# Performance work log

Measured on AMD Instinct MI355X. Metric: run time of the kernel, lower is better.

The kernel has to match this reference:

```python
import jax, jax.numpy as jnp
import numpy as np

N_NODES = 50000
N_EDGES = 800000
D_IN = 96
D_OUT = 96
NEG_SLOPE = 0.2


def setup_inputs() -> dict:
    key = jax.random.key(0)
    k1, k2, k3, k4, k5 = jax.random.split(key, 5)
    x = jax.random.normal(k1, (N_NODES, D_IN), dtype=jnp.float32)
    W = jax.random.normal(k2, (D_IN, D_OUT), dtype=jnp.float32) * (1.0 / np.sqrt(D_IN))
    att_src = jax.random.normal(k3, (D_OUT,), dtype=jnp.float32) * 0.1
    att_dst = jax.random.normal(k4, (D_OUT,), dtype=jnp.float32) * 0.1
    bias = jnp.zeros((D_OUT,), dtype=jnp.float32)
    edge_index = jax.random.randint(k5, (2, N_EDGES), 0, N_NODES, dtype=jnp.int64)
    return {"x": x, "W": W, "att_src": att_src, "att_dst": att_dst,
            "bias": bias, "edge_index": edge_index}


def reference(x, W, att_src, att_dst, bias, edge_index):
    N = x.shape[0]
    # Linear transform: h = x W   [N, D_out]
    h = x @ W
    # PyG GATConv default add_self_loops=True
    loops = jnp.arange(N, dtype=edge_index.dtype)
    src = jnp.concatenate([edge_index[0], loops])  # message source j
    dst = jnp.concatenate([edge_index[1], loops])  # aggregation target i
    # Per-node attention halves, gathered per edge
    a_src = h @ att_src  # [N]
    a_dst = h @ att_dst  # [N]
    e = jax.nn.leaky_relu(a_src[src] + a_dst[dst], NEG_SLOPE)  # [E+N]
    # Segment softmax over edges sharing the same destination
    m = jax.ops.segment_max(e, dst, num_segments=N)  # every node has a self-loop
    e = jnp.exp(e - m[dst])
    denom = jax.ops.segment_sum(e, dst, num_segments=N)
    alpha = e / (denom[dst] + 1e-16)  # [E+N]
    # Weighted scatter-aggregate of source features
    out = jax.ops.segment_sum(h[src] * alpha[:, None], dst, num_segments=N)
    return jnp.tanh(out + bias)
```

## Files before the change

### kernel.cpp

```cpp
#include <hip/hip_runtime.h>
#include <hip/hip_bf16.h>
#include <cstdint>

#define N_NODES 50000
#define N_EDGES 800000
#define D 96
#define NEG_SLOPE 0.2f
#define R1ROWS 16
#define BUCKET 64
#define NXCD 8
#define DST_PER_PART (N_NODES / NXCD)

__global__ __launch_bounds__(384) void k1_gemm(
    const float* __restrict__ x, const float* __restrict__ W,
    __hip_bfloat16* __restrict__ hb) {
    __shared__ float Ws[D][D];
    __shared__ float xs[R1ROWS][D];
    const int tx = threadIdx.x, ty = threadIdx.y;
    const int t = ty * 96 + tx;
    const size_t row0 = (size_t)blockIdx.x * R1ROWS;

    {
        const float4* W4 = (const float4*)W;
        float4* Ws4 = (float4*)Ws;
#pragma unroll
        for (int i = 0; i < 6; ++i) Ws4[t + 384 * i] = W4[t + 384 * i];
        const float4* x4 = (const float4*)(x + row0 * D);
        ((float4*)xs)[t] = x4[t];
    }
    __syncthreads();

    float acc0 = 0.f, acc1 = 0.f, acc2 = 0.f, acc3 = 0.f;
#pragma unroll
    for (int k = 0; k < D; k += 4) {
        float4 xa = *(const float4*)&xs[ty][k];
        float4 xb = *(const float4*)&xs[ty + 4][k];
        float4 xc = *(const float4*)&xs[ty + 8][k];
        float4 xd = *(const float4*)&xs[ty + 12][k];
        float w0 = Ws[k][tx], w1 = Ws[k + 1][tx], w2 = Ws[k + 2][tx], w3 = Ws[k + 3][tx];
        acc0 += xa.x * w0 + xa.y * w1 + xa.z * w2 + xa.w * w3;
        acc1 += xb.x * w0 + xb.y * w1 + xb.z * w2 + xb.w * w3;
        acc2 += xc.x * w0 + xc.y * w1 + xc.z * w2 + xc.w * w3;
        acc3 += xd.x * w0 + xd.y * w1 + xd.z * w2 + xd.w * w3;
    }
    hb[(row0 + ty     ) * D + tx] = __float2bfloat16(acc0);
    hb[(row0 + ty + 4 ) * D + tx] = __float2bfloat16(acc1);
    hb[(row0 + ty + 8 ) * D + tx] = __float2bfloat16(acc2);
    hb[(row0 + ty + 12) * D + tx] = __float2bfloat16(acc3);
}

__global__ __launch_bounds__(256) void k1b_att(
    const __hip_bfloat16* __restrict__ hb, const float* __restrict__ att_src,
    const float* __restrict__ att_dst, float* __restrict__ a_src,
    float* __restrict__ a_dst, int* __restrict__ cnt) {
    const int lane = threadIdx.x & 63;
    const int row = (blockIdx.x * 256 + threadIdx.x) >> 6;
    if (row >= N_NODES) return;
    float s = 0.f, d = 0.f;
    if (lane < 48) {
        uint hv = ((const uint*)hb)[(size_t)row * 48 + lane];
        float h0 = __uint_as_float(hv << 16);
        float h1 = __uint_as_float(hv & 0xffff0000u);
        float2 as = *(const float2*)(att_src + lane * 2);
        float2 ad = *(const float2*)(att_dst + lane * 2);
        s = h0 * as.x + h1 * as.y;
        d = h0 * ad.x + h1 * ad.y;
    }
#pragma unroll
    for (int off = 32; off >= 1; off >>= 1) {
        s += __shfl_down(s, off);
        d += __shfl_down(d, off);
    }
    if (lane == 0) { a_src[row] = s; a_dst[row] = d; cnt[row] = 0; }
}

__global__ void k_bucket(const int* __restrict__ ei,
                         const float* __restrict__ a_src, const float* __restrict__ a_dst,
                         int* __restrict__ cnt, uint* __restrict__ bkt) {
    const int part = blockIdx.x & (NXCD - 1);
    const int e = (blockIdx.x >> 3) * 256 + threadIdx.x;
    if (e >= N_EDGES) return;
    int d = ei[N_EDGES + e];
    int lo = part * DST_PER_PART;
    if (d < lo || d >= lo + DST_PER_PART) return;
    int s = ei[e];
    float v = a_src[s] + a_dst[d];
    v = v > 0.f ? v : NEG_SLOPE * v;
    float w = __expf(v);
    uint u = __float_as_uint(w);
    uint wb = (u + 0x7FFFu + ((u >> 16) & 1u)) & 0xFFFF0000u;
    uint pk = wb | (uint)s;
    int pos = atomicAdd(&cnt[d], 1);
    if (pos < BUCKET) bkt[(size_t)d * BUCKET + pos] = pk;
}

__global__ __launch_bounds__(256) void k_gather(
    const int* __restrict__ cnt, const uint* __restrict__ bkt,
    const float* __restrict__ a_src, const float* __restrict__ a_dst,
    const __hip_bfloat16* __restrict__ hb, const float* __restrict__ bias,
    float* __restrict__ out) {
    const uint lane = threadIdx.x & 63;
    const uint ll = (lane < 48u) ? lane : (lane - 16u);
    const int part = blockIdx.x & (NXCD - 1);
    const int l = (int)((blockIdx.x >> 3) * 4 + (threadIdx.x >> 6));
    if (l >= DST_PER_PART) return;
    const int node = part * DST_PER_PART + l;
    const uint* __restrict__ hbu = (const uint*)hb;
    const uint* __restrict__ bucket = bkt + (size_t)node * BUCKET;
    const int cn = min(cnt[node], BUCKET);

    float es = a_src[node] + a_dst[node];
    es = es > 0.f ? es : NEG_SLOPE * es;
    float wself = __expf(es);
    uint pself = hbu[(uint)node * 48u + ll];
    float acc0 = __uint_as_float(pself << 16) * wself;
    float acc1 = __uint_as_float(pself & 0xffff0000u) * wself;
    float wsum = wself;

    int k = 0;
    for (; k + 15 < cn; k += 16) {
        uint b[16];
        *(uint4*)&b[0]  = *(const uint4*)&bucket[k];
        *(uint4*)&b[4]  = *(const uint4*)&bucket[k + 4];
        *(uint4*)&b[8]  = *(const uint4*)&bucket[k + 8];
        *(uint4*)&b[12] = *(const uint4*)&bucket[k + 12];
        uint p[16];
#pragma unroll
        for (int j = 0; j < 16; ++j) p[j] = hbu[(b[j] & 0xFFFFu) * 48u + ll];
#pragma unroll
        for (int j = 0; j < 16; ++j) {
            float w = __uint_as_float(b[j] & 0xFFFF0000u);
            acc0 += __uint_as_float(p[j] << 16) * w;
            acc1 += __uint_as_float(p[j] & 0xffff0000u) * w;
            wsum += w;
        }
    }
    if (k + 7 < cn) {
        uint b[8];
        *(uint4*)&b[0] = *(const uint4*)&bucket[k];
        *(uint4*)&b[4] = *(const uint4*)&bucket[k + 4];
        uint p[8];
#pragma unroll
        for (int j = 0; j < 8; ++j) p[j] = hbu[(b[j] & 0xFFFFu) * 48u + ll];
#pragma unroll
        for (int j = 0; j < 8; ++j) {
            float w = __uint_as_float(b[j] & 0xFFFF0000u);
            acc0 += __uint_as_float(p[j] << 16) * w;
            acc1 += __uint_as_float(p[j] & 0xffff0000u) * w;
            wsum += w;
        }
        k += 8;
    }
    if (k + 3 < cn) {
        uint b[4];
        *(uint4*)&b[0] = *(const uint4*)&bucket[k];
        uint p[4];
#pragma unroll
        for (int j = 0; j < 4; ++j) p[j] = hbu[(b[j] & 0xFFFFu) * 48u + ll];
#pragma unroll
        for (int j = 0; j < 4; ++j) {
            float w = __uint_as_float(b[j] & 0xFFFF0000u);
            acc0 += __uint_as_float(p[j] << 16) * w;
            acc1 += __uint_as_float(p[j] & 0xffff0000u) * w;
            wsum += w;
        }
        k += 4;
    }
    for (; k < cn; ++k) {
        uint e0 = bucket[k];
        uint p0 = hbu[(e0 & 0xFFFFu) * 48u + ll];
        float w0 = __uint_as_float(e0 & 0xFFFF0000u);
        acc0 += __uint_as_float(p0 << 16) * w0;
        acc1 += __uint_as_float(p0 & 0xffff0000u) * w0;
        wsum += w0;
    }

    if (lane < 48) {
        float inv = 1.f / (wsum + 1e-16f);
        float2 bv = *(const float2*)(bias + lane * 2);
        float2 o;
        o.x = tanhf(acc0 * inv + bv.x);
        o.y = tanhf(acc1 * inv + bv.y);
        *(float2*)(out + (size_t)node * D + lane * 2) = o;
    }
}

extern "C" void kernel_launch(void* const* d_in, const int* in_sizes, int n_in,
                              void* d_out, int out_size, void* d_ws, size_t ws_size,
                              hipStream_t stream) {
    const float* x       = (const float*)d_in[0];
    const float* W       = (const float*)d_in[1];
    const float* att_src = (const float*)d_in[2];
    const float* att_dst = (const float*)d_in[3];
    const float* bias    = (const float*)d_in[4];
    const int*   ei      = (const int*)d_in[5];
    float* out = (float*)d_out;

    char* ws = (char*)d_ws;
    __hip_bfloat16* hb = (__hip_bfloat16*)ws; ws += (size_t)N_NODES * D * 2;
    float* a_src  = (float*)ws; ws += (size_t)N_NODES * 4;
    float* a_dst  = (float*)ws; ws += (size_t)N_NODES * 4;
    int*   cnt    = (int*)ws;   ws += (size_t)N_NODES * 4;
    uint*  bkt    = (uint*)ws;  ws += (size_t)N_NODES * BUCKET * 4;

    k1_gemm<<<N_NODES / R1ROWS, dim3(96, 4), 0, stream>>>(x, W, hb);
    k1b_att<<<(N_NODES * 64 + 255) / 256, 256, 0, stream>>>(hb, att_src, att_dst, a_src, a_dst, cnt);
    k_bucket<<<((N_EDGES + 255) / 256) * NXCD, 256, 0, stream>>>(ei, a_src, a_dst, cnt, bkt);
    k_gather<<<((DST_PER_PART + 3) / 4) * NXCD, 256, 0, stream>>>(
        cnt, bkt, a_src, a_dst, hb, bias, out);
}
```

Measured before the change: 114.1 us.

## Store 16-bit source ids in buckets and compute edge weights in gather

The bucketing kernel now writes only a 16-bit source index per edge instead of a packed bf16 weight plus index, and skips the a_src/a_dst gathers and exp there. The gather kernel recomputes the leaky-relu/exp weight per edge from a_src[s] plus a cached a_dst, which also gives full fp32 weight precision. This halves bucket memory traffic and removes random loads from the bucketing pass. In exchange, every lane now does a redundant a_src gather and exp per edge, and 16-bit ids cannot represent node indices above 65535, though N=50000 fits.

Measured after the change: 115.8 us. About the same (+1.4%).

```diff
diff --git a/kernel.cpp b/kernel.cpp
--- a/kernel.cpp
+++ b/kernel.cpp
@@ -74,28 +74,20 @@
     if (lane == 0) { a_src[row] = s; a_dst[row] = d; cnt[row] = 0; }
 }
 
-__global__ void k_bucket(const int* __restrict__ ei,
-                         const float* __restrict__ a_src, const float* __restrict__ a_dst,
-                         int* __restrict__ cnt, uint* __restrict__ bkt) {
+__global__ void k_bucket(const int* __restrict__ ei, int* __restrict__ cnt,
+                         ushort* __restrict__ bkt) {
     const int part = blockIdx.x & (NXCD - 1);
     const int e = (blockIdx.x >> 3) * 256 + threadIdx.x;
     if (e >= N_EDGES) return;
     int d = ei[N_EDGES + e];
     int lo = part * DST_PER_PART;
     if (d < lo || d >= lo + DST_PER_PART) return;
-    int s = ei[e];
-    float v = a_src[s] + a_dst[d];
-    v = v > 0.f ? v : NEG_SLOPE * v;
-    float w = __expf(v);
-    uint u = __float_as_uint(w);
-    uint wb = (u + 0x7FFFu + ((u >> 16) & 1u)) & 0xFFFF0000u;
-    uint pk = wb | (uint)s;
     int pos = atomicAdd(&cnt[d], 1);
-    if (pos < BUCKET) bkt[(size_t)d * BUCKET + pos] = pk;
+    if (pos < BUCKET) bkt[(size_t)d * BUCKET + pos] = (ushort)ei[e];
 }
 
 __global__ __launch_bounds__(256) void k_gather(
-    const int* __restrict__ cnt, const uint* __restrict__ bkt,
+    const int* __restrict__ cnt, const ushort* __restrict__ bkt,
     const float* __restrict__ a_src, const float* __restrict__ a_dst,
     const __hip_bfloat16* __restrict__ hb, const float* __restrict__ bias,
     float* __restrict__ out) {
@@ -106,10 +98,11 @@
     if (l >= DST_PER_PART) return;
     const int node = part * DST_PER_PART + l;
     const uint* __restrict__ hbu = (const uint*)hb;
-    const uint* __restrict__ bucket = bkt + (size_t)node * BUCKET;
+    const ushort* __restrict__ bucket = bkt + (size_t)node * BUCKET;
     const int cn = min(cnt[node], BUCKET);
-
-    float es = a_src[node] + a_dst[node];
+    const float adst = a_dst[node];
+
+    float es = a_src[node] + adst;
     es = es > 0.f ? es : NEG_SLOPE * es;
     float wself = __expf(es);
     uint pself = hbu[(uint)node * 48u + ll];
@@ -119,32 +112,49 @@
 
     int k = 0;
     for (; k + 15 < cn; k += 16) {
-        uint b[16];
-        *(uint4*)&b[0]  = *(const uint4*)&bucket[k];
-        *(uint4*)&b[4]  = *(const uint4*)&bucket[k + 4];
-        *(uint4*)&b[8]  = *(const uint4*)&bucket[k + 8];
-        *(uint4*)&b[12] = *(const uint4*)&bucket[k + 12];
-        uint p[16];
-#pragma unroll
-        for (int j = 0; j < 16; ++j) p[j] = hbu[(b[j] & 0xFFFFu) * 48u + ll];
+        uint4 b0 = *(const uint4*)&bucket[k];
+        uint4 b1 = *(const uint4*)&bucket[k + 8];
+        uint s[16];
+        s[0] = b0.x & 0xFFFFu;  s[1] = b0.x >> 16;
+        s[2] = b0.y & 0xFFFFu;  s[3] = b0.y >> 16;
+        s[4] = b0.z & 0xFFFFu;  s[5] = b0.z >> 16;
+        s[6] = b0.w & 0xFFFFu;  s[7] = b0.w >> 16;
+        s[8] = b1.x & 0xFFFFu;  s[9] = b1.x >> 16;
+        s[10] = b1.y & 0xFFFFu; s[11] = b1.y >> 16;
+        s[12] = b1.z & 0xFFFFu; s[13] = b1.z >> 16;
+        s[14] = b1.w & 0xFFFFu; s[15] = b1.w >> 16;
+        uint p[16]; float a[16];
+#pragma unroll
+        for (int j = 0; j < 16; ++j) p[j] = hbu[s[j] * 48u + ll];
+#pragma unroll
+        for (int j = 0; j < 16; ++j) a[j] = a_src[s[j]];
 #pragma unroll
         for (int j = 0; j < 16; ++j) {
-            float w = __uint_as_float(b[j] & 0xFFFF0000u);
+            float v = a[j] + adst;
+            v = v > 0.f ? v : NEG_SLOPE * v;
+            float w = __expf(v);
             acc0 += __uint_as_float(p[j] << 16) * w;
             acc1 += __uint_as_float(p[j] & 0xffff0000u) * w;
             wsum += w;
         }
     }
     if (k + 7 < cn) {
-        uint b[8];
-        *(uint4*)&b[0] = *(const uint4*)&bucket[k];
-        *(uint4*)&b[4] = *(const uint4*)&bucket[k + 4];
-        uint p[8];
-#pragma unroll
-        for (int j = 0; j < 8; ++j) p[j] = hbu[(b[j] & 0xFFFFu) * 48u + ll];
+        uint4 b0 = *(const uint4*)&bucket[k];
+        uint s[8];
+        s[0] = b0.x & 0xFFFFu; s[1] = b0.x >> 16;
+        s[2] = b0.y & 0xFFFFu; s[3] = b0.y >> 16;
+        s[4] = b0.z & 0xFFFFu; s[5] = b0.z >> 16;
+        s[6] = b0.w & 0xFFFFu; s[7] = b0.w >> 16;
+        uint p[8]; float a[8];
+#pragma unroll
+        for (int j = 0; j < 8; ++j) p[j] = hbu[s[j] * 48u + ll];
+#pragma unroll
+        for (int j = 0; j < 8; ++j) a[j] = a_src[s[j]];
 #pragma unroll
         for (int j = 0; j < 8; ++j) {
-            float w = __uint_as_float(b[j] & 0xFFFF0000u);
+            float v = a[j] + adst;
+            v = v > 0.f ? v : NEG_SLOPE * v;
+            float w = __expf(v);
             acc0 += __uint_as_float(p[j] << 16) * w;
             acc1 += __uint_as_float(p[j] & 0xffff0000u) * w;
             wsum += w;
@@ -152,14 +162,20 @@
         k += 8;
     }
     if (k + 3 < cn) {
-        uint b[4];
-        *(uint4*)&b[0] = *(const uint4*)&bucket[k];
-        uint p[4];
-#pragma unroll
-        for (int j = 0; j < 4; ++j) p[j] = hbu[(b[j] & 0xFFFFu) * 48u + ll];
+        uint2 b0 = *(const uint2*)&bucket[k];
+        uint s[4];
+        s[0] = b0.x & 0xFFFFu; s[1] = b0.x >> 16;
+        s[2] = b0.y & 0xFFFFu; s[3] = b0.y >> 16;
+        uint p[4]; float a[4];
+#pragma unroll
+        for (int j = 0; j < 4; ++j) p[j] = hbu[s[j] * 48u + ll];
+#pragma unroll
+        for (int j = 0; j < 4; ++j) a[j] = a_src[s[j]];
 #pragma unroll
         for (int j = 0; j < 4; ++j) {
-            float w = __uint_as_float(b[j] & 0xFFFF0000u);
+            float v = a[j] + adst;
+            v = v > 0.f ? v : NEG_SLOPE * v;
+            float w = __expf(v);
             acc0 += __uint_as_float(p[j] << 16) * w;
             acc1 += __uint_as_float(p[j] & 0xffff0000u) * w;
             wsum += w;
@@ -167,9 +183,11 @@
         k += 4;
     }
     for (; k < cn; ++k) {
-        uint e0 = bucket[k];
-        uint p0 = hbu[(e0 & 0xFFFFu) * 48u + ll];
-        float w0 = __uint_as_float(e0 & 0xFFFF0000u);
+        uint s0 = bucket[k];
+        uint p0 = hbu[s0 * 48u + ll];
+        float v = a_src[s0] + adst;
+        v = v > 0.f ? v : NEG_SLOPE * v;
+        float w0 = __expf(v);
         acc0 += __uint_as_float(p0 << 16) * w0;
         acc1 += __uint_as_float(p0 & 0xffff0000u) * w0;
         wsum += w0;
@@ -198,14 +216,14 @@
 
     char* ws = (char*)d_ws;
     __hip_bfloat16* hb = (__hip_bfloat16*)ws; ws += (size_t)N_NODES * D * 2;
-    float* a_src  = (float*)ws; ws += (size_t)N_NODES * 4;
-    float* a_dst  = (float*)ws; ws += (size_t)N_NODES * 4;
-    int*   cnt    = (int*)ws;   ws += (size_t)N_NODES * 4;
-    uint*  bkt    = (uint*)ws;  ws += (size_t)N_NODES * BUCKET * 4;
+    float*  a_src = (float*)ws;  ws += (size_t)N_NODES * 4;
+    float*  a_dst = (float*)ws;  ws += (size_t)N_NODES * 4;
+    int*    cnt   = (int*)ws;    ws += (size_t)N_NODES * 4;
+    ushort* bkt   = (ushort*)ws; ws += (size_t)N_NODES * BUCKET * 2;
 
     k1_gemm<<<N_NODES / R1ROWS, dim3(96, 4), 0, stream>>>(x, W, hb);
     k1b_att<<<(N_NODES * 64 + 255) / 256, 256, 0, stream>>>(hb, att_src, att_dst, a_src, a_dst, cnt);
-    k_bucket<<<((N_EDGES + 255) / 256) * NXCD, 256, 0, stream>>>(ei, a_src, a_dst, cnt, bkt);
+    k_bucket<<<((N_EDGES + 255) / 256) * NXCD, 256, 0, stream>>>(ei, cnt, bkt);
     k_gather<<<((DST_PER_PART + 3) / 4) * NXCD, 256, 0, stream>>>(
         cnt, bkt, a_src, a_dst, hb, bias, out);
 }
```
